# Kernel optimization log

Measured on AMD Instinct MI355X. Metric: run time of the kernel, lower is better.

## Reference

```python
import jax, jax.numpy as jnp
import numpy as np

B, S, D, H = 4, 2048, 1024, 16
DH = D // H  # 64


def setup_inputs() -> dict:
    key = jax.random.key(0)
    ks = jax.random.split(key, 7)
    scale = 1.0 / np.sqrt(DH)  # ~ torch Linear init scale
    return {
        "seqs": jax.random.normal(ks[0], (B, S, D), dtype=jnp.float32),
        "Wq": jax.random.normal(ks[1], (H, DH, DH), dtype=jnp.float32) * scale,
        "bq": jax.random.normal(ks[2], (H, DH), dtype=jnp.float32) * scale,
        "Wk": jax.random.normal(ks[3], (H, DH, DH), dtype=jnp.float32) * scale,
        "bk": jax.random.normal(ks[4], (H, DH), dtype=jnp.float32) * scale,
        "Wv": jax.random.normal(ks[5], (H, DH, DH), dtype=jnp.float32) * scale,
        "bv": jax.random.normal(ks[6], (H, DH), dtype=jnp.float32) * scale,
    }


def reference(seqs, Wq, bq, Wk, bk, Wv, bv):
    # seqs: [B, S, D] -> per-head slices [B, S, H, DH]
    x = seqs.reshape(B, S, H, DH)
    # torch Linear: y = s @ W.T + b  (W: [out, in]) -> einsum over 'in' axis d
    q = jnp.einsum("bshd,hed->bshe", x, Wq) + bq  # [B,S,H,DH]
    k = jnp.einsum("bshd,hed->bshe", x, Wk) + bk
    v = jnp.einsum("bshd,hed->bshe", x, Wv) + bv
    inv_sqrt = 1.0 / jnp.sqrt(jnp.asarray(DH, dtype=seqs.dtype))
    scores = jnp.einsum("bshe,bthe->bhst", q, k) * inv_sqrt  # [B,H,S,S]
    attn = jax.nn.softmax(scores, axis=-1)
    out = jnp.einsum("bhst,bthe->bshe", attn, v)  # [B,S,H,DH]
    # torch.hstack over heads == concat along feature dim
    return out.reshape(B, S, D)
```

## Files before the change

### kernel.cpp

```cpp
#include <hip/hip_runtime.h>
#include <hip/hip_bf16.h>

#define NB 4
#define NS 2048
#define ND 1024
#define NH 16
#define NDH 64
#define SCF 0.18033688011112042f

typedef __attribute__((ext_vector_type(8))) short bf16x8;
typedef __attribute__((ext_vector_type(4))) float f32x4;

__device__ __forceinline__ float bf2f(unsigned short u) {
    union { unsigned int u; float f; } x; x.u = ((unsigned int)u) << 16; return x.f;
}
__device__ __forceinline__ unsigned short f2bf(float f) {
    union { float f; unsigned int u; } x; x.f = f;
    unsigned int r = x.u + 0x7FFFu + ((x.u >> 16) & 1u);
    return (unsigned short)(r >> 16);
}
__device__ __forceinline__ unsigned short f2bf_fast(float f) {
    union { float f; unsigned int u; } x; x.f = f;
    return (unsigned short)((x.u + 0x8000u) >> 16);
}
__device__ __forceinline__ unsigned int pkbf(float a, float b) {
    union { float f; unsigned int u; } x, y; x.f = a; y.f = b;
    return __builtin_amdgcn_perm(y.u + 0x8000u, x.u + 0x8000u, 0x07060302u);
}
__device__ __forceinline__ unsigned int pktr(float a, float b) {
    union { float f; unsigned int u; } x, y; x.f = a; y.f = b;
    return __builtin_amdgcn_perm(y.u, x.u, 0x07060302u);
}
__device__ __forceinline__ void gl_lds16(const unsigned short* g, unsigned short* l) {
    __builtin_amdgcn_global_load_lds(
        (const __attribute__((address_space(1))) void*)g,
        (__attribute__((address_space(3))) void*)l, 16, 0, 0);
}

__global__ __launch_bounds__(256) void convert_w_kernel(
    const unsigned short* __restrict__ x,
    const void* __restrict__ Wq, const void* __restrict__ bq,
    const void* __restrict__ Wk, const void* __restrict__ bk,
    const void* __restrict__ Wv, const void* __restrict__ bv,
    int* __restrict__ flag,
    unsigned short* __restrict__ Wb,
    unsigned short* __restrict__ Bb)
{
    __shared__ int sflag;
    const int tid = threadIdx.x;
    if (tid < 64) {
        int bad = 0, zer = 0;
        for (int i = tid; i < 1024; i += 64) {
            const unsigned short u = x[2 * i];
            const int e = (u >> 7) & 0xFF;
            if (e >= 0x8F) bad++;
            if (e == 0 && (u & 0x7F)) bad++;
            if (u == 0) zer++;
        }
        #pragma unroll
        for (int off = 1; off < 64; off <<= 1) {
            bad += __shfl_xor(bad, off, 64);
            zer += __shfl_xor(zer, off, 64);
        }
        if (tid == 0) {
            const int f = (bad > 64 || zer > 512) ? 1 : 0;
            sflag = f;
            flag[0] = f;
        }
    }
    __syncthreads();
    const int isf32 = sflag;

    const void* Wsrc[3] = { Wq, Wk, Wv };
    const void* Bsrc[3] = { bq, bk, bv };
    const int NW = 3 * 65536, NBIAS = 3 * 1024;
    for (int i = blockIdx.x * blockDim.x + tid; i < NW + NBIAS;
         i += gridDim.x * blockDim.x) {
        int m, off; const void* src; unsigned short* dst;
        if (i < NW) { m = i >> 16; off = i & 65535; src = Wsrc[m]; dst = Wb + i; }
        else { int j = i - NW; m = j >> 10; off = j & 1023; src = Bsrc[m];
               dst = Bb + j; }
        float v = isf32 ? ((const float*)src)[off]
                        : bf2f(((const unsigned short*)src)[off]);
        if (m == 0) v *= SCF;
        *dst = f2bf(v);
    }
}

__global__ __launch_bounds__(256) void qkv_proj_kernel(
    const unsigned short* __restrict__ x,
    const unsigned short* __restrict__ Wb,
    const unsigned short* __restrict__ Bb,
    const int* __restrict__ flag,
    unsigned short* __restrict__ Qw, unsigned short* __restrict__ Kw,
    unsigned short* __restrict__ VwT)
{
    __shared__ __align__(16) unsigned short Tl[3 * 64 * 72];
    __shared__ __align__(16) unsigned short Xs[64 * 72];

    const int isf32 = flag[0];
    const int tid  = threadIdx.x;
    const int wave = tid >> 6, lane = tid & 63;
    const int quad = lane >> 4, l16 = lane & 15;
    const int ttile = blockIdx.x, h = blockIdx.y;
    const int b  = ttile >> 5;
    const int s0 = (ttile & 31) * 64;
    const int bh = b * NH + h;

    if (isf32) {
        const float* xb = (const float*)x + (size_t)(ttile * 64) * ND + h * NDH;
        #pragma unroll
        for (int p = 0; p < 4; ++p) {
            const int c = p * 256 + tid;
            const int row = c >> 4, cc = c & 15;
            const f32x4 v = *(const f32x4*)(xb + (size_t)row * ND + cc * 4);
            uint2 d; d.x = pkbf(v[0], v[1]); d.y = pkbf(v[2], v[3]);
            *(uint2*)(Xs + row * 72 + cc * 4) = d;
        }
    } else {
        const unsigned short* xb = x + (size_t)(ttile * 64) * ND + h * NDH;
        #pragma unroll
        for (int p = 0; p < 2; ++p) {
            const int c = p * 256 + tid;
            const int row = c >> 3, cc = c & 7;
            *(bf16x8*)(Xs + row * 72 + cc * 8) =
                *(const bf16x8*)(xb + (size_t)row * ND + cc * 8);
        }
    }
    __syncthreads();

    const int xr = (wave * 16 + l16) * 72;
    const bf16x8 af0 = *(const bf16x8*)(Xs + xr + quad * 8);
    const bf16x8 af1 = *(const bf16x8*)(Xs + xr + 32 + quad * 8);

    #pragma unroll
    for (int m = 0; m < 3; ++m) {
        const unsigned short* W = Wb + m * 65536 + h * 4096;
        unsigned short* R = Tl + m * (64 * 72);
        #pragma unroll
        for (int n = 0; n < 4; ++n) {
            const unsigned short* wrow = W + (n * 16 + l16) * NDH;
            const bf16x8 b0 = *(const bf16x8*)(wrow + quad * 8);
            const bf16x8 b1 = *(const bf16x8*)(wrow + 32 + quad * 8);
            f32x4 acc = {0.f, 0.f, 0.f, 0.f};
            acc = __builtin_amdgcn_mfma_f32_16x16x32_bf16(af0, b0, acc, 0, 0, 0);
            acc = __builtin_amdgcn_mfma_f32_16x16x32_bf16(af1, b1, acc, 0, 0, 0);
            const float bias = bf2f(Bb[m * 1024 + h * NDH + n * 16 + l16]);
            if (m < 2) {
                #pragma unroll
                for (int r = 0; r < 4; ++r) {
                    const int row = wave * 16 + quad * 4 + r;
                    R[row * 72 + n * 16 + l16] = f2bf_fast(acc[r] + bias);
                }
            } else {
                #pragma unroll
                for (int r = 0; r < 4; ++r) {
                    const int tok = wave * 16 + quad * 4 + r;
                    const int pc = ((tok & 15) << 2) | (tok >> 4);
                    R[(n * 16 + l16) * 72 + pc] = f2bf_fast(acc[r] + bias);
                }
            }
        }
    }
    __syncthreads();
    #pragma unroll
    for (int p = 0; p < 2; ++p) {
        const int ch = tid + p * 256;
        const int tl = ch >> 3, sub = ch & 7;
        *(bf16x8*)(Qw + ((size_t)bh * NS + s0 + tl) * NDH + sub * 8) =
            *(const bf16x8*)(Tl + tl * 72 + sub * 8);
        *(bf16x8*)(Kw + ((size_t)bh * NS + s0 + tl) * NDH + sub * 8) =
            *(const bf16x8*)(Tl + 64 * 72 + tl * 72 + sub * 8);
        *(bf16x8*)(VwT + ((size_t)bh * NDH + tl) * NS + s0 + sub * 8) =
            *(const bf16x8*)(Tl + 2 * 64 * 72 + tl * 72 + sub * 8);
    }
}

#define STAGE(tt, buf) do {                                                        \
    const unsigned short* kg = Kb + (size_t)(tt) * 4096 + (wave * 16 + lr) * 64 + lc; \
    const unsigned short* vg = Vb + (size_t)(wave * 16 + lr) * NS + (tt) * 64 + lc;   \
    unsigned short* kl = smem + (buf) * 4096 + wave * 1024;                        \
    unsigned short* vl = smem + 8192 + (buf) * 4096 + wave * 1024;                 \
    gl_lds16(kg,                 kl);                                              \
    gl_lds16(kg + 8 * 64,        kl + 512);                                        \
    gl_lds16(vg,                 vl);                                              \
    gl_lds16(vg + (size_t)8 * NS, vl + 512);                                       \
} while (0)

__global__ __launch_bounds__(256, 2) void attn_kernel(
    const unsigned short* __restrict__ Qw,
    const unsigned short* __restrict__ Kw,
    const unsigned short* __restrict__ VwT,
    const int* __restrict__ flag,
    unsigned short* __restrict__ out)
{
    __shared__ __align__(16) unsigned short smem[34816];
    unsigned short* Ot = smem;

    const int isf32 = flag[0];
    const int tid  = threadIdx.x;
    const int wave = tid >> 6, lane = tid & 63;
    const int quad = lane >> 4, l16 = lane & 15;
    const int bh = blockIdx.x & 63;
    const int qt = blockIdx.x >> 6;
    const int b = bh >> 4, h = bh & 15;

    const unsigned short* Qb = Qw  + (size_t)bh * NS * NDH;
    const unsigned short* Kb = Kw  + (size_t)bh * NS * NDH;
    const unsigned short* Vb = VwT + (size_t)bh * NDH * NS;

    unsigned short* PtW = smem + 16384 + wave * (4 * 1152);

    const int lr = lane >> 3;
    const int lc = ((lane & 7) ^ lr) << 3;

    const int rsw = (l16 & 7) << 3;
    const int c0 = (quad * 8) ^ rsw;
    const int c1 = (quad * 8 + 32) ^ rsw;

    bf16x8 qf[4][2];
    #pragma unroll
    for (int mh = 0; mh < 4; ++mh) {
        const int tok = qt * 256 + wave * 64 + mh * 16 + l16;
        qf[mh][0] = *(const bf16x8*)(Qb + (size_t)tok * NDH + quad * 8);
        qf[mh][1] = *(const bf16x8*)(Qb + (size_t)tok * NDH + 32 + quad * 8);
    }

    f32x4 o[4][4];
    float os[4][4];
    #pragma unroll
    for (int mh = 0; mh < 4; ++mh) {
        #pragma unroll
        for (int n = 0; n < 4; ++n) o[mh][n] = f32x4{0.f, 0.f, 0.f, 0.f};
        #pragma unroll
        for (int r = 0; r < 4; ++r) os[mh][r] = 0.f;
    }

    STAGE(0, 0);

    #pragma unroll 1
    for (int t = 0; t < NS / 64; ++t) {
        __syncthreads();
        if (t + 1 < NS / 64) STAGE(t + 1, (t + 1) & 1);

        const unsigned short* KB = smem + (t & 1) * 4096;
        const unsigned short* VB = smem + 8192 + (t & 1) * 4096;

        bf16x8 kb[4][2], vb[4][2];
        #pragma unroll
        for (int n = 0; n < 4; ++n) {
            const int ro = (n * 16 + l16) * 64;
            kb[n][0] = *(const bf16x8*)(KB + ro + c0);
            kb[n][1] = *(const bf16x8*)(KB + ro + c1);
            vb[n][0] = *(const bf16x8*)(VB + ro + c0);
            vb[n][1] = *(const bf16x8*)(VB + ro + c1);
        }

        #pragma unroll
        for (int mh = 0; mh < 4; ++mh) {
            unsigned short* Pm = PtW + mh * 1152;
            f32x4 sf[4];
            #pragma unroll
            for (int n = 0; n < 4; ++n) {
                f32x4 acc = {0.f, 0.f, 0.f, 0.f};
                acc = __builtin_amdgcn_mfma_f32_16x16x32_bf16(qf[mh][0], kb[n][0], acc, 0, 0, 0);
                acc = __builtin_amdgcn_mfma_f32_16x16x32_bf16(qf[mh][1], kb[n][1], acc, 0, 0, 0);
                sf[n] = acc;
            }
            #pragma unroll
            for (int r = 0; r < 4; ++r) {
                const float p0 = __builtin_amdgcn_exp2f(sf[0][r]);
                const float p1 = __builtin_amdgcn_exp2f(sf[1][r]);
                const float p2 = __builtin_amdgcn_exp2f(sf[2][r]);
                const float p3 = __builtin_amdgcn_exp2f(sf[3][r]);
                os[mh][r] += (p0 + p1) + (p2 + p3);
                uint2 d; d.x = pktr(p0, p1); d.y = pktr(p2, p3);
                *(uint2*)(Pm + (quad * 4 + r) * 72 + l16 * 4) = d;
            }
            const bf16x8 pa0 = *(const bf16x8*)(Pm + l16 * 72 + quad * 8);
            const bf16x8 pa1 = *(const bf16x8*)(Pm + l16 * 72 + 32 + quad * 8);
            #pragma unroll
            for (int n = 0; n < 4; ++n) {
                o[mh][n] = __builtin_amdgcn_mfma_f32_16x16x32_bf16(pa0, vb[n][0], o[mh][n], 0, 0, 0);
                o[mh][n] = __builtin_amdgcn_mfma_f32_16x16x32_bf16(pa1, vb[n][1], o[mh][n], 0, 0, 0);
            }
        }
    }

    float inv[4][4];
    #pragma unroll
    for (int mh = 0; mh < 4; ++mh) {
        #pragma unroll
        for (int r = 0; r < 4; ++r) {
            float s = os[mh][r];
            #pragma unroll
            for (int off = 1; off < 16; off <<= 1)
                s += __shfl_xor(s, off, 64);
            inv[mh][r] = 1.0f / s;
        }
    }

    if (isf32) {
        float* of = (float*)out;
        #pragma unroll
        for (int mh = 0; mh < 4; ++mh) {
            #pragma unroll
            for (int r = 0; r < 4; ++r) {
                const int s = qt * 256 + wave * 64 + mh * 16 + quad * 4 + r;
                #pragma unroll
                for (int n = 0; n < 4; ++n)
                    of[((size_t)(b * NS + s)) * ND + h * NDH + n * 16 + l16] =
                        o[mh][n][r] * inv[mh][r];
            }
        }
    } else {
        __syncthreads();
        #pragma unroll
        for (int mh = 0; mh < 4; ++mh) {
            #pragma unroll
            for (int r = 0; r < 4; ++r) {
                const int row = wave * 64 + mh * 16 + quad * 4 + r;
                #pragma unroll
                for (int n = 0; n < 4; ++n)
                    Ot[row * 72 + n * 16 + l16] = f2bf(o[mh][n][r] * inv[mh][r]);
            }
        }
        __syncthreads();
        #pragma unroll
        for (int p = 0; p < 8; ++p) {
            const int ch = tid + p * 256;
            const int tl = ch >> 3, sub = ch & 7;
            const int s = qt * 256 + tl;
            *(bf16x8*)(out + ((size_t)(b * NS + s)) * ND + h * NDH + sub * 8) =
                *(const bf16x8*)(Ot + tl * 72 + sub * 8);
        }
    }
}

extern "C" void kernel_launch(void* const* d_in, const int* in_sizes, int n_in,
                              void* d_out, int out_size, void* d_ws, size_t ws_size,
                              hipStream_t stream)
{
    const unsigned short* x = (const unsigned short*)d_in[0];
    int* flag = (int*)d_ws;
    const size_t per = (size_t)NB * NH * NS * NDH;
    unsigned short* Qw  = (unsigned short*)((char*)d_ws + 256);
    unsigned short* Kw  = Qw + per;
    unsigned short* VwT = Kw + per;
    unsigned short* Wb  = VwT + per;
    unsigned short* Bb  = Wb + 3 * 65536;

    convert_w_kernel<<<256, 256, 0, stream>>>(
        x, d_in[1], d_in[2], d_in[3], d_in[4], d_in[5], d_in[6], flag, Wb, Bb);
    qkv_proj_kernel<<<dim3(NB * NS / 64, NH), 256, 0, stream>>>(
        x, Wb, Bb, flag, Qw, Kw, VwT);
    attn_kernel<<<NB * NH * (NS / 256), 256, 0, stream>>>(
        Qw, Kw, VwT, flag, (unsigned short*)d_out);
}
```

Measured before the change: 193.1 us.

## Compute transposed S and O tiles to keep P in registers, skipping LDS

Swaps the MFMA operand order so the score and output accumulators come out transposed. Each lane then holds the probabilities in the layout the PV MFMA needs as its B operand, so P no longer goes through LDS. To make this work, the V^T columns are re-permuted in the projection kernel. The change drops the per-tile P stores and loads, shrinks LDS (which may allow more blocks per CU), and reduces the row-sum shuffle reduction. The risk is that the token permutation must exactly match the register packing order, or results will be wrong.

Result: faster. 187.1 us, median of 2 (-3.1%).

```diff
diff --git a/kernel.cpp b/kernel.cpp
--- a/kernel.cpp
+++ b/kernel.cpp
@@ -156,7 +156,8 @@
                 #pragma unroll
                 for (int r = 0; r < 4; ++r) {
                     const int tok = wave * 16 + quad * 4 + r;
-                    const int pc = ((tok & 15) << 2) | (tok >> 4);
+                    const int pc = (tok & 32) | (((tok >> 2) & 3) << 3)
+                                 | (((tok >> 4) & 1) << 2) | (tok & 3);
                     R[(n * 16 + l16) * 72 + pc] = f2bf_fast(acc[r] + bias);
                 }
             }
@@ -194,7 +195,7 @@
     const int* __restrict__ flag,
     unsigned short* __restrict__ out)
 {
-    __shared__ __align__(16) unsigned short smem[34816];
+    __shared__ __align__(16) unsigned short smem[18432];
     unsigned short* Ot = smem;
 
     const int isf32 = flag[0];
@@ -209,8 +210,6 @@
     const unsigned short* Kb = Kw  + (size_t)bh * NS * NDH;
     const unsigned short* Vb = VwT + (size_t)bh * NDH * NS;
 
-    unsigned short* PtW = smem + 16384 + wave * (4 * 1152);
-
     const int lr = lane >> 3;
     const int lc = ((lane & 7) ^ lr) << 3;
 
@@ -227,13 +226,12 @@
     }
 
     f32x4 o[4][4];
-    float os[4][4];
+    float os[4];
     #pragma unroll
     for (int mh = 0; mh < 4; ++mh) {
         #pragma unroll
         for (int n = 0; n < 4; ++n) o[mh][n] = f32x4{0.f, 0.f, 0.f, 0.f};
-        #pragma unroll
-        for (int r = 0; r < 4; ++r) os[mh][r] = 0.f;
+        os[mh] = 0.f;
     }
 
     STAGE(0, 0);
@@ -258,71 +256,69 @@
 
         #pragma unroll
         for (int mh = 0; mh < 4; ++mh) {
-            unsigned short* Pm = PtW + mh * 1152;
             f32x4 sf[4];
             #pragma unroll
             for (int n = 0; n < 4; ++n) {
                 f32x4 acc = {0.f, 0.f, 0.f, 0.f};
-                acc = __builtin_amdgcn_mfma_f32_16x16x32_bf16(qf[mh][0], kb[n][0], acc, 0, 0, 0);
-                acc = __builtin_amdgcn_mfma_f32_16x16x32_bf16(qf[mh][1], kb[n][1], acc, 0, 0, 0);
+                acc = __builtin_amdgcn_mfma_f32_16x16x32_bf16(kb[n][0], qf[mh][0], acc, 0, 0, 0);
+                acc = __builtin_amdgcn_mfma_f32_16x16x32_bf16(kb[n][1], qf[mh][1], acc, 0, 0, 0);
                 sf[n] = acc;
             }
-            #pragma unroll
-            for (int r = 0; r < 4; ++r) {
-                const float p0 = __builtin_amdgcn_exp2f(sf[0][r]);
-                const float p1 = __builtin_amdgcn_exp2f(sf[1][r]);
-                const float p2 = __builtin_amdgcn_exp2f(sf[2][r]);
-                const float p3 = __builtin_amdgcn_exp2f(sf[3][r]);
-                os[mh][r] += (p0 + p1) + (p2 + p3);
-                uint2 d; d.x = pktr(p0, p1); d.y = pktr(p2, p3);
-                *(uint2*)(Pm + (quad * 4 + r) * 72 + l16 * 4) = d;
-            }
-            const bf16x8 pa0 = *(const bf16x8*)(Pm + l16 * 72 + quad * 8);
-            const bf16x8 pa1 = *(const bf16x8*)(Pm + l16 * 72 + 32 + quad * 8);
-            #pragma unroll
-            for (int n = 0; n < 4; ++n) {
-                o[mh][n] = __builtin_amdgcn_mfma_f32_16x16x32_bf16(pa0, vb[n][0], o[mh][n], 0, 0, 0);
-                o[mh][n] = __builtin_amdgcn_mfma_f32_16x16x32_bf16(pa1, vb[n][1], o[mh][n], 0, 0, 0);
-            }
-        }
-    }
-
-    float inv[4][4];
+            float pv[4][4];
+            #pragma unroll
+            for (int n = 0; n < 4; ++n) {
+                pv[n][0] = __builtin_amdgcn_exp2f(sf[n][0]);
+                pv[n][1] = __builtin_amdgcn_exp2f(sf[n][1]);
+                pv[n][2] = __builtin_amdgcn_exp2f(sf[n][2]);
+                pv[n][3] = __builtin_amdgcn_exp2f(sf[n][3]);
+                os[mh] += (pv[n][0] + pv[n][1]) + (pv[n][2] + pv[n][3]);
+            }
+            union { bf16x8 v; unsigned int d[4]; } pa0, pa1;
+            pa0.d[0] = pktr(pv[0][0], pv[0][1]); pa0.d[1] = pktr(pv[0][2], pv[0][3]);
+            pa0.d[2] = pktr(pv[1][0], pv[1][1]); pa0.d[3] = pktr(pv[1][2], pv[1][3]);
+            pa1.d[0] = pktr(pv[2][0], pv[2][1]); pa1.d[1] = pktr(pv[2][2], pv[2][3]);
+            pa1.d[2] = pktr(pv[3][0], pv[3][1]); pa1.d[3] = pktr(pv[3][2], pv[3][3]);
+            #pragma unroll
+            for (int n = 0; n < 4; ++n) {
+                o[mh][n] = __builtin_amdgcn_mfma_f32_16x16x32_bf16(vb[n][0], pa0.v, o[mh][n], 0, 0, 0);
+                o[mh][n] = __builtin_amdgcn_mfma_f32_16x16x32_bf16(vb[n][1], pa1.v, o[mh][n], 0, 0, 0);
+            }
+        }
+    }
+
+    float inv[4];
     #pragma unroll
     for (int mh = 0; mh < 4; ++mh) {
-        #pragma unroll
-        for (int r = 0; r < 4; ++r) {
-            float s = os[mh][r];
-            #pragma unroll
-            for (int off = 1; off < 16; off <<= 1)
-                s += __shfl_xor(s, off, 64);
-            inv[mh][r] = 1.0f / s;
-        }
+        float s = os[mh];
+        s += __shfl_xor(s, 16, 64);
+        s += __shfl_xor(s, 32, 64);
+        inv[mh] = 1.0f / s;
     }
 
     if (isf32) {
         float* of = (float*)out;
         #pragma unroll
         for (int mh = 0; mh < 4; ++mh) {
-            #pragma unroll
-            for (int r = 0; r < 4; ++r) {
-                const int s = qt * 256 + wave * 64 + mh * 16 + quad * 4 + r;
-                #pragma unroll
-                for (int n = 0; n < 4; ++n)
-                    of[((size_t)(b * NS + s)) * ND + h * NDH + n * 16 + l16] =
-                        o[mh][n][r] * inv[mh][r];
+            const size_t base =
+                ((size_t)(b * NS + qt * 256 + wave * 64 + mh * 16 + l16)) * ND + h * NDH;
+            #pragma unroll
+            for (int n = 0; n < 4; ++n) {
+                f32x4 v = { o[mh][n][0] * inv[mh], o[mh][n][1] * inv[mh],
+                            o[mh][n][2] * inv[mh], o[mh][n][3] * inv[mh] };
+                *(f32x4*)(of + base + n * 16 + quad * 4) = v;
             }
         }
     } else {
         __syncthreads();
         #pragma unroll
         for (int mh = 0; mh < 4; ++mh) {
-            #pragma unroll
-            for (int r = 0; r < 4; ++r) {
-                const int row = wave * 64 + mh * 16 + quad * 4 + r;
+            const int row = wave * 64 + mh * 16 + l16;
+            #pragma unroll
+            for (int n = 0; n < 4; ++n) {
                 #pragma unroll
-                for (int n = 0; n < 4; ++n)
-                    Ot[row * 72 + n * 16 + l16] = f2bf(o[mh][n][r] * inv[mh][r]);
+                for (int r = 0; r < 4; ++r)
+                    Ot[row * 72 + n * 16 + quad * 4 + r] =
+                        f2bf(o[mh][n][r] * inv[mh]);
             }
         }
         __syncthreads();
```
